# Performance work log

Measured on AMD Instinct MI355X. Metric: run time of the kernel, lower is better.

## Reference

```python
import jax, jax.numpy as jnp
import numpy as np

LAMBDA_POS = 0.5
LAMBDA_RAD = 0.5
LAMBDA_UNPAIR = 0.5
EPS = 1e-6
N_PRED = 20


def setup_inputs() -> dict:
    key = jax.random.key(0)
    k1, k2 = jax.random.split(key)
    B, L = 1000000, 12
    pred = jax.random.uniform(k1, (B, N_PRED, 4), dtype=jnp.float32)
    label = jax.random.uniform(k2, (B, L, 4), dtype=jnp.float32)
    return {"pred": pred, "label": label}


def reference(pred, label):
    # pred: [B, 20, 4] (x, y, radius, prob); label: [B, L, 4]
    B, L = label.shape[0], label.shape[1]
    yl = label[:, :, None, :]   # [B, L, 1, 4]
    yp = pred[:, None, :, :]    # [B, 1, 20, 4]
    dist = jnp.sqrt((yl[..., 0] - yp[..., 0]) ** 2 + (yl[..., 1] - yp[..., 1]) ** 2)  # [B, L, 20]
    rdiff = jnp.abs(yl[..., 2] - yp[..., 2])  # [B, L, 20]
    cost = LAMBDA_POS * dist + LAMBDA_RAD * rdiff  # [B, L, 20]
    idx = jnp.argmin(cost, axis=-1)  # [B, L]

    matched = jnp.take_along_axis(pred, idx[:, :, None], axis=1)  # [B, L, 4]
    mdist = jnp.sqrt((label[..., 0] - matched[..., 0]) ** 2 + (label[..., 1] - matched[..., 1]) ** 2)
    mrdiff = jnp.abs(label[..., 2] - matched[..., 2])
    prob_pair = -jnp.log(matched[..., 3] + EPS)  # prob_loss(p, 1)
    loss_pair = jnp.sum(LAMBDA_POS * mdist + LAMBDA_RAD * mrdiff + prob_pair, axis=-1)  # [B]

    # pair_mask[i] = 1 if any label matched pred i
    mask = jnp.zeros((B, N_PRED), dtype=pred.dtype)
    mask = mask.at[jnp.arange(B)[:, None], idx].set(1.0)

    unpair_term = (-jnp.log(1.0 - pred[..., 3] + EPS) + LAMBDA_RAD * pred[..., 2]) * LAMBDA_UNPAIR  # [B, 20]
    loss_unpair = jnp.sum((1.0 - mask) * unpair_term, axis=-1)  # [B]

    return loss_pair / L + loss_unpair / (N_PRED - L)
```

## Files before the change

kernel.cpp:

```cpp
#include <hip/hip_runtime.h>
#include <math.h>

constexpr int NP = 20;
constexpr int NL = 12;

__device__ __forceinline__ float fast_log(float x) {
    return __builtin_amdgcn_logf(x) * 0.69314718055994530942f;
}

__global__ __launch_bounds__(256) void myloss_kernel(
    const float4* __restrict__ pred,
    const float4* __restrict__ label,
    float* __restrict__ out,
    int B)
{
    int b = blockIdx.x * blockDim.x + threadIdx.x;
    if (b >= B) return;

    const float4* p4 = pred  + (size_t)b * NP;
    const float4* l4 = label + (size_t)b * NL;

    float px[NP], py[NP], pr[NP], pq[NP];
#pragma unroll
    for (int j = 0; j < NP; ++j) {
        float4 v = p4[j];
        px[j] = v.x; py[j] = v.y; pr[j] = v.z; pq[j] = v.w;
    }

    float lp = 0.0f;
    unsigned mask = 0u;
#pragma unroll 2
    for (int l = 0; l < NL; ++l) {
        float4 lv = l4[l];
        float    bs[4];
        float    bq[4];
        unsigned bb[4];
#pragma unroll
        for (int c = 0; c < 4; ++c) { bs[c] = INFINITY; bq[c] = 0.0f; bb[c] = 0u; }
#pragma unroll
        for (int i = 0; i < 5; ++i) {
#pragma unroll
            for (int c = 0; c < 4; ++c) {
                int p = c * 5 + i;
                float s;
                {
#pragma clang fp contract(off)
                    float dx = lv.x - px[p];
                    float dy = lv.y - py[p];
                    float d2 = dx * dx + dy * dy;
                    float dist = sqrtf(d2);
                    s = dist + fabsf(lv.z - pr[p]);
                }
                bool lt = s < bs[c];
                bs[c] = lt ? s : bs[c];
                bq[c] = lt ? pq[p] : bq[c];
                bb[c] = lt ? (1u << p) : bb[c];
            }
        }
        bool m01 = bs[1] < bs[0];
        float sa = m01 ? bs[1] : bs[0];
        float qa = m01 ? bq[1] : bq[0];
        unsigned ba = m01 ? bb[1] : bb[0];
        bool m23 = bs[3] < bs[2];
        float sb = m23 ? bs[3] : bs[2];
        float qb = m23 ? bq[3] : bq[2];
        unsigned bbm = m23 ? bb[3] : bb[2];
        bool mf = sb < sa;
        float sm = mf ? sb : sa;
        float qm = mf ? qb : qa;
        unsigned bm = mf ? bbm : ba;

        lp += 0.5f * sm - fast_log(qm + 1e-6f);
        mask |= bm;
    }

    float lu = 0.0f;
#pragma unroll
    for (int p = 0; p < NP; ++p) {
        float t = (-fast_log(1.0f - pq[p] + 1e-6f) + 0.5f * pr[p]) * 0.5f;
        lu += (mask & (1u << p)) ? 0.0f : t;
    }

    out[b] = lp * (1.0f / 12.0f) + lu * 0.125f;
}

extern "C" void kernel_launch(void* const* d_in, const int* in_sizes, int n_in,
                              void* d_out, int out_size, void* d_ws, size_t ws_size,
                              hipStream_t stream) {
    const float4* pred  = (const float4*)d_in[0];
    const float4* label = (const float4*)d_in[1];
    float* out = (float*)d_out;
    int B = out_size;
    int threads = 256;
    int blocks = (B + threads - 1) / threads;
    hipLaunchKernelGGL(myloss_kernel, dim3(blocks), dim3(threads), 0, stream,
                       pred, label, out, B);
}
```

Before: 607.7 us.

## Use fast approximate sqrt/FMA for argmin with exact fallback on near-ties

The main argmin pass now uses a fused multiply-add and the hardware approximate sqrt, while also tracking the second-best cost. When the best and second-best costs fall within a small tolerance, it recomputes the argmin exactly with the original non-contracted arithmetic in a sequential loop. This cuts ALU cost in the hot loop while keeping the selected index consistent with the reference. It also adds min/max bookkeeping, a rarely taken divergent branch, and a minimum-occupancy hint in the launch bounds that may constrain register allocation.

```diff
diff --git a/kernel.cpp b/kernel.cpp
--- a/kernel.cpp
+++ b/kernel.cpp
@@ -8,7 +8,7 @@
     return __builtin_amdgcn_logf(x) * 0.69314718055994530942f;
 }
 
-__global__ __launch_bounds__(256) void myloss_kernel(
+__global__ __launch_bounds__(256, 4) void myloss_kernel(
     const float4* __restrict__ pred,
     const float4* __restrict__ label,
     float* __restrict__ out,
@@ -29,19 +29,50 @@
 
     float lp = 0.0f;
     unsigned mask = 0u;
+
 #pragma unroll 2
     for (int l = 0; l < NL; ++l) {
         float4 lv = l4[l];
-        float    bs[4];
-        float    bq[4];
-        unsigned bb[4];
+
+        float m1[4], m2[4], mq[4];
+        unsigned mb[4];
 #pragma unroll
-        for (int c = 0; c < 4; ++c) { bs[c] = INFINITY; bq[c] = 0.0f; bb[c] = 0u; }
+        for (int c = 0; c < 4; ++c) { m1[c] = INFINITY; m2[c] = INFINITY; mq[c] = 0.0f; mb[c] = 0u; }
+
 #pragma unroll
         for (int i = 0; i < 5; ++i) {
 #pragma unroll
             for (int c = 0; c < 4; ++c) {
                 int p = c * 5 + i;
+                float dx = lv.x - px[p];
+                float dy = lv.y - py[p];
+                float d2 = __builtin_fmaf(dy, dy, dx * dx);
+                float dist = __builtin_amdgcn_sqrtf(d2);
+                float s = dist + fabsf(lv.z - pr[p]);
+                m2[c] = fminf(m2[c], fmaxf(m1[c], s));
+                bool lt = s < m1[c];
+                m1[c] = lt ? s : m1[c];
+                mq[c] = lt ? pq[p] : mq[c];
+                mb[c] = lt ? (1u << p) : mb[c];
+            }
+        }
+
+        float g1 = m1[0], g2 = m2[0], qm = mq[0];
+        unsigned bm = mb[0];
+#pragma unroll
+        for (int c = 1; c < 4; ++c) {
+            g2 = fminf(fmaxf(g1, m1[c]), fminf(g2, m2[c]));
+            bool sel = m1[c] < g1;
+            g1 = sel ? m1[c] : g1;
+            qm = sel ? mq[c] : qm;
+            bm = sel ? mb[c] : bm;
+        }
+
+        if (g2 - g1 < 4e-6f) {
+            float sm = INFINITY, qq = 0.0f;
+            unsigned bb = 0u;
+#pragma unroll 1
+            for (int p = 0; p < NP; ++p) {
                 float s;
                 {
 #pragma clang fp contract(off)
@@ -51,26 +82,15 @@
                     float dist = sqrtf(d2);
                     s = dist + fabsf(lv.z - pr[p]);
                 }
-                bool lt = s < bs[c];
-                bs[c] = lt ? s : bs[c];
-                bq[c] = lt ? pq[p] : bq[c];
-                bb[c] = lt ? (1u << p) : bb[c];
+                bool ltp = s < sm;
+                sm = ltp ? s : sm;
+                qq = ltp ? pq[p] : qq;
+                bb = ltp ? (1u << p) : bb;
             }
+            g1 = sm; qm = qq; bm = bb;
         }
-        bool m01 = bs[1] < bs[0];
-        float sa = m01 ? bs[1] : bs[0];
-        float qa = m01 ? bq[1] : bq[0];
-        unsigned ba = m01 ? bb[1] : bb[0];
-        bool m23 = bs[3] < bs[2];
-        float sb = m23 ? bs[3] : bs[2];
-        float qb = m23 ? bq[3] : bq[2];
-        unsigned bbm = m23 ? bb[3] : bb[2];
-        bool mf = sb < sa;
-        float sm = mf ? sb : sa;
-        float qm = mf ? qb : qa;
-        unsigned bm = mf ? bbm : ba;
 
-        lp += 0.5f * sm - fast_log(qm + 1e-6f);
+        lp += 0.5f * g1 - fast_log(qm + 1e-6f);
         mask |= bm;
     }
 
```

Result: slower. 1.019 ms (+67.7%).
